# Kernel tuning notes

Measured on AMD Instinct MI355X. Metric: run time of the kernel, lower is better.

Reference implementation:

```python
import math
import jax, jax.numpy as jnp
import numpy as np

N_HEADS = 8

def setup_inputs() -> dict:
    key = jax.random.key(0)
    bs, n_heads, ch, l = 4, N_HEADS, 64, 1024
    width = 3 * n_heads * ch      # 1536 (packed q,k,v channels)
    T = 3 * l                     # 3072 (three spatial bands: ll, lh, hl)
    qkv = jax.random.normal(key, (bs, width, T), dtype=jnp.float32)
    return {"qkv": qkv, "l": l}

def reference(qkv, l):
    n_heads = N_HEADS
    bs, width, T = qkv.shape
    ch = width // (3 * n_heads)
    q, k, v = jnp.split(qkv, 3, axis=1)              # each (bs, n_heads*ch, T)
    scale = 1.0 / math.sqrt(math.sqrt(ch))
    qh = (q * scale).reshape(bs * n_heads, ch, T)
    kh = (k * scale).reshape(bs * n_heads, ch, T)
    vh = v.reshape(bs * n_heads, ch, T)
    # The original computes attention separately for q[:, :, :l], [l:2l], [2l:],
    # but k/v (and the softmax axis s) are identical, so computing attention
    # over the full query once and splitting the output is the same math.
    attn = jnp.einsum('bct,bcs->bts', qh, kh)        # (bs*H, T, T)
    w = jax.nn.softmax(attn.astype(jnp.float32), axis=-1).astype(attn.dtype)
    agg = jnp.einsum('bts,bcs->bct', w, vh).reshape(bs, n_heads * ch, T)
    return (agg[:, :, :l], agg[:, :, l:2 * l], agg[:, :, 2 * l:])
```

## Files before the change

### kernel.cpp

```cpp
#include <hip/hip_runtime.h>
#include <hip/hip_bf16.h>
#include <stdint.h>

#define T      3072
#define CH     64
#define HEADS  32
#define BM     128
#define BN     64
#define NIT    (T / BN)
#define PSTR   72

typedef unsigned short u16;
typedef short short8 __attribute__((ext_vector_type(8)));
typedef float floatx4 __attribute__((ext_vector_type(4)));

__device__ __forceinline__ unsigned pk2(float a, float b) {
  union { __hip_bfloat162 h; unsigned u; } cv;
  cv.h = __float22bfloat162_rn(float2{a, b});
  return cv.u;
}

__device__ __forceinline__ void gl_lds16(const void* g, void* l) {
  __builtin_amdgcn_global_load_lds(
      (const __attribute__((address_space(1))) uint32_t*)g,
      (__attribute__((address_space(3))) uint32_t*)l, 16, 0, 0);
}

__global__ __launch_bounds__(256) void qktrans(
    const float* __restrict__ qkv, u16* __restrict__ Qt, u16* __restrict__ Kt) {
  __shared__ __align__(16) u16 tl[64][PSTR];
  const int ttile = blockIdx.x, hh = blockIdx.y, role = blockIdx.z;
  const int b = hh >> 3, h = hh & 7;
  const int t0 = ttile * 64;
  const int tid = threadIdx.x;
  const float* src = qkv + (size_t)(b * 1536 + role * 512 + h * CH) * T;
  const float scale = (role == 0) ? 0.18033688011112042f : 1.0f;

#pragma unroll
  for (int p = 0; p < 2; ++p) {
    const int c0 = p * 32 + ((tid >> 4) << 1);
    const int ts = (tid & 15) * 4;
    float4 a = *(const float4*)(src + (size_t)c0 * T + t0 + ts);
    float4 c = *(const float4*)(src + (size_t)(c0 + 1) * T + t0 + ts);
    *(unsigned*)&tl[ts + 0][c0] = pk2(a.x * scale, c.x * scale);
    *(unsigned*)&tl[ts + 1][c0] = pk2(a.y * scale, c.y * scale);
    *(unsigned*)&tl[ts + 2][c0] = pk2(a.z * scale, c.z * scale);
    *(unsigned*)&tl[ts + 3][c0] = pk2(a.w * scale, c.w * scale);
  }
  __syncthreads();
  u16* dst = (role == 0 ? Qt : Kt) + (size_t)hh * T * CH;
#pragma unroll
  for (int q = 0; q < 2; ++q) {
    const int t = q * 32 + (tid >> 3);
    const int cc = (tid & 7) * 8;
    uint4 v = *(const uint4*)&tl[t][cc];
    *(uint4*)(dst + (size_t)(t0 + t) * CH + cc) = v;
  }
}

__global__ __launch_bounds__(256) void vcast(
    const float* __restrict__ qkv, u16* __restrict__ Vo) {
  const int b = blockIdx.y;
  const size_t i = ((size_t)blockIdx.x * 256 + threadIdx.x) * 8;
  const float4* s4 = (const float4*)(qkv + (size_t)b * 1536 * T + (size_t)1024 * T + i);
  float4 a = s4[0], c = s4[1];
  uint4 o;
  o.x = pk2(a.x, a.y); o.y = pk2(a.z, a.w);
  o.z = pk2(c.x, c.y); o.w = pk2(c.z, c.w);
  *(uint4*)(Vo + (size_t)b * 512 * T + i) = o;
}

__global__ __launch_bounds__(256, 3) void attn(
    const u16* __restrict__ Qt, const u16* __restrict__ Kt,
    const u16* __restrict__ Vg, float* __restrict__ out) {
  __shared__ __align__(16) u16 KB[2][BN * CH];
  __shared__ __align__(16) u16 VB[2][CH * BN];
  __shared__ __align__(16) u16 PL[4][32 * PSTR];

  const int qtile = blockIdx.x, hh = blockIdx.y;
  const int tid = threadIdx.x;
  const int wave = tid >> 6, lane = tid & 63;
  const int l15 = lane & 15, quad = lane >> 4;
  const int t0 = qtile * BM + wave * 32;

  const u16* Qh = Qt + (size_t)hh * T * CH;
  const u16* Kh = Kt + (size_t)hh * T * CH;
  const u16* Vh = Vg + (size_t)hh * CH * T;

  short8 qf[2][2];
#pragma unroll
  for (int tq = 0; tq < 2; ++tq)
#pragma unroll
    for (int kc = 0; kc < 2; ++kc)
      qf[tq][kc] = *(const short8*)(Qh + (size_t)(t0 + tq * 16 + l15) * CH + kc * 32 + quad * 8);

  floatx4 oacc[2][4] = {};
  float lsum[2][2] = {};

  int srow[2], scb[2];
#pragma unroll
  for (int j = 0; j < 2; ++j) {
    const int p = wave * 128 + j * 64 + lane;
    srow[j] = p >> 3;
    scb[j]  = (p & 7) ^ ((srow[j] + 2 * (srow[j] >> 3)) & 7);
  }
  const int swl = (l15 + 2 * (l15 >> 3)) & 7;
  u16* plw = PL[wave];

#define STAGE(buf, s0)                                                              \
  do {                                                                              \
    _Pragma("unroll")                                                               \
    for (int j = 0; j < 2; ++j)                                                     \
      gl_lds16(Kh + (size_t)((s0) + srow[j]) * CH + scb[j] * 8,                     \
               &KB[buf][(wave * 128 + j * 64) * 8]);                                \
    _Pragma("unroll")                                                               \
    for (int j = 0; j < 2; ++j)                                                     \
      gl_lds16(Vh + (size_t)srow[j] * T + (s0) + scb[j] * 8,                        \
               &VB[buf][(wave * 128 + j * 64) * 8]);                                \
  } while (0)

  STAGE(0, 0);

  for (int it = 0; it < NIT; ++it) {
    const int cur = it & 1;
    __syncthreads();
    if (it + 1 < NIT) STAGE(cur ^ 1, (it + 1) * BN);

    const u16* KL = KB[cur];
    const u16* VL = VB[cur];

    floatx4 sacc[2][4];
#pragma unroll
    for (int nt = 0; nt < 4; ++nt) {
      const int ph0 = quad ^ swl ^ ((nt & 1) * 4);
      const int base = (nt * 16 + l15) * CH;
      const short8 kf0 = *(const short8*)(KL + base + ph0 * 8);
      const short8 kf1 = *(const short8*)(KL + base + (ph0 ^ 4) * 8);
#pragma unroll
      for (int tq = 0; tq < 2; ++tq) {
        floatx4 z = {0.f, 0.f, 0.f, 0.f};
        z = __builtin_amdgcn_mfma_f32_16x16x32_bf16(kf0, qf[tq][0], z, 0, 0, 0);
        z = __builtin_amdgcn_mfma_f32_16x16x32_bf16(kf1, qf[tq][1], z, 0, 0, 0);
        sacc[tq][nt] = z;
      }
    }

#pragma unroll
    for (int tq = 0; tq < 2; ++tq)
#pragma unroll
      for (int nt = 0; nt < 4; ++nt) {
        floatx4 sv = sacc[tq][nt];
        float p0 = __builtin_amdgcn_exp2f(sv[0]);
        float p1 = __builtin_amdgcn_exp2f(sv[1]);
        float p2 = __builtin_amdgcn_exp2f(sv[2]);
        float p3 = __builtin_amdgcn_exp2f(sv[3]);
        lsum[tq][nt & 1] += (p0 + p1) + (p2 + p3);
        uint2 w; w.x = pk2(p0, p1); w.y = pk2(p2, p3);
        *(uint2*)(plw + (l15 + tq * 16) * PSTR + nt * 16 + quad * 4) = w;
      }

#pragma unroll
    for (int ks = 0; ks < 2; ++ks) {
      short8 pf0 = *(const short8*)(plw + l15 * PSTR + ks * 32 + quad * 8);
      short8 pf1 = *(const short8*)(plw + (l15 + 16) * PSTR + ks * 32 + quad * 8);
#pragma unroll
      for (int mt = 0; mt < 4; ++mt) {
        const int ph = quad ^ swl ^ ((mt & 1) * 4) ^ (ks * 4);
        const short8 vf = *(const short8*)(VL + (mt * 16 + l15) * BN + ph * 8);
        oacc[0][mt] = __builtin_amdgcn_mfma_f32_16x16x32_bf16(pf0, vf, oacc[0][mt], 0, 0, 0);
        oacc[1][mt] = __builtin_amdgcn_mfma_f32_16x16x32_bf16(pf1, vf, oacc[1][mt], 0, 0, 0);
      }
    }
  }

  float ls[2];
#pragma unroll
  for (int tq = 0; tq < 2; ++tq) {
    float s = lsum[tq][0] + lsum[tq][1];
    s += __shfl_xor(s, 16, 64);
    s += __shfl_xor(s, 32, 64);
    ls[tq] = s;
  }
  float linv[2][4];
#pragma unroll
  for (int tq = 0; tq < 2; ++tq)
#pragma unroll
    for (int r = 0; r < 4; ++r)
      linv[tq][r] = 1.0f / __shfl(ls[tq], quad * 4 + r, 64);

  const int b = hh >> 3, h = hh & 7;
#pragma unroll
  for (int tq = 0; tq < 2; ++tq) {
    const int tg = t0 + tq * 16 + quad * 4;
    const int band = tg >> 10, tt = tg & 1023;
    float* obase = out + (size_t)band * (4 * 512 * 1024)
                       + (size_t)b * (512 * 1024)
                       + (size_t)(h * CH) * 1024 + tt;
#pragma unroll
    for (int mt = 0; mt < 4; ++mt) {
      const int c = mt * 16 + l15;
      float4 v;
      v.x = oacc[tq][mt][0] * linv[tq][0];
      v.y = oacc[tq][mt][1] * linv[tq][1];
      v.z = oacc[tq][mt][2] * linv[tq][2];
      v.w = oacc[tq][mt][3] * linv[tq][3];
      *(float4*)(obase + (size_t)c * 1024) = v;
    }
  }
}

extern "C" void kernel_launch(void* const* d_in, const int* in_sizes, int n_in,
                              void* d_out, int out_size, void* d_ws, size_t ws_size,
                              hipStream_t stream) {
  (void)in_sizes; (void)n_in; (void)out_size; (void)ws_size;
  const float* qkv = (const float*)d_in[0];
  u16* Qt = (u16*)d_ws;
  u16* Kt = Qt + (size_t)HEADS * T * CH;
  u16* Vo = Kt + (size_t)HEADS * T * CH;
  float* out = (float*)d_out;

  qktrans<<<dim3(T / 64, HEADS, 2), 256, 0, stream>>>(qkv, Qt, Kt);
  vcast<<<dim3(768, 4), 256, 0, stream>>>(qkv, Vo);
  attn<<<dim3(T / BM, HEADS), 256, 0, stream>>>(Qt, Kt, Vo, out);
}
```

Baseline: 220.4 us.

## Keep softmax probabilities in registers via permlane swaps and fuse V cast

The exponentiated scores are packed to bf16 and rearranged across lanes with permlane32/permlane16 swaps to form the MFMA A-operand directly. This removes the per-iteration write and read of P through shared memory and drops the PL buffer. Separately, the V fp32-to-bf16 cast is folded into the Q/K transpose kernel as a third grid role, saving one launch. The register remap must match the MFMA operand layout exactly, and the swaps add cross-lane instructions.

```diff
diff --git a/kernel.cpp b/kernel.cpp
--- a/kernel.cpp
+++ b/kernel.cpp
@@ -8,7 +8,6 @@
 #define BM     128
 #define BN     64
 #define NIT    (T / BN)
-#define PSTR   72
 
 typedef unsigned short u16;
 typedef short short8 __attribute__((ext_vector_type(8)));
@@ -26,13 +25,49 @@
       (__attribute__((address_space(3))) uint32_t*)l, 16, 0, 0);
 }
 
+__device__ __forceinline__ void pl32swap(unsigned& x, unsigned& y) {
+#if __has_builtin(__builtin_amdgcn_permlane32_swap)
+  auto r = __builtin_amdgcn_permlane32_swap(x, y, false, false);
+  x = r[0]; y = r[1];
+#else
+  asm("v_permlane32_swap_b32 %0, %1" : "+v"(x), "+v"(y));
+#endif
+}
+__device__ __forceinline__ void pl16swap(unsigned& x, unsigned& y) {
+#if __has_builtin(__builtin_amdgcn_permlane16_swap)
+  auto r = __builtin_amdgcn_permlane16_swap(x, y, false, false);
+  x = r[0]; y = r[1];
+#else
+  asm("v_permlane16_swap_b32 %0, %1" : "+v"(x), "+v"(y));
+#endif
+}
+
 __global__ __launch_bounds__(256) void qktrans(
-    const float* __restrict__ qkv, u16* __restrict__ Qt, u16* __restrict__ Kt) {
-  __shared__ __align__(16) u16 tl[64][PSTR];
+    const float* __restrict__ qkv, u16* __restrict__ Qt, u16* __restrict__ Kt,
+    u16* __restrict__ Vo) {
+  __shared__ __align__(16) u16 tl[64][72];
   const int ttile = blockIdx.x, hh = blockIdx.y, role = blockIdx.z;
   const int b = hh >> 3, h = hh & 7;
   const int t0 = ttile * 64;
   const int tid = threadIdx.x;
+
+  if (role == 2) {
+    const float* vsrc = qkv + (size_t)(b * 1536 + 1024 + h * CH) * T;
+    u16* vdst = Vo + (size_t)(b * 512 + h * CH) * T;
+#pragma unroll
+    for (int p = 0; p < 2; ++p) {
+      const int r = p * 32 + (tid >> 3);
+      const int off = (tid & 7) * 8;
+      const float4* s4 = (const float4*)(vsrc + (size_t)r * T + t0 + off);
+      float4 a = s4[0], c = s4[1];
+      uint4 o;
+      o.x = pk2(a.x, a.y); o.y = pk2(a.z, a.w);
+      o.z = pk2(c.x, c.y); o.w = pk2(c.z, c.w);
+      *(uint4*)(vdst + (size_t)r * T + t0 + off) = o;
+    }
+    return;
+  }
+
   const float* src = qkv + (size_t)(b * 1536 + role * 512 + h * CH) * T;
   const float scale = (role == 0) ? 0.18033688011112042f : 1.0f;
 
@@ -58,24 +93,11 @@
   }
 }
 
-__global__ __launch_bounds__(256) void vcast(
-    const float* __restrict__ qkv, u16* __restrict__ Vo) {
-  const int b = blockIdx.y;
-  const size_t i = ((size_t)blockIdx.x * 256 + threadIdx.x) * 8;
-  const float4* s4 = (const float4*)(qkv + (size_t)b * 1536 * T + (size_t)1024 * T + i);
-  float4 a = s4[0], c = s4[1];
-  uint4 o;
-  o.x = pk2(a.x, a.y); o.y = pk2(a.z, a.w);
-  o.z = pk2(c.x, c.y); o.w = pk2(c.z, c.w);
-  *(uint4*)(Vo + (size_t)b * 512 * T + i) = o;
-}
-
 __global__ __launch_bounds__(256, 3) void attn(
     const u16* __restrict__ Qt, const u16* __restrict__ Kt,
     const u16* __restrict__ Vg, float* __restrict__ out) {
   __shared__ __align__(16) u16 KB[2][BN * CH];
   __shared__ __align__(16) u16 VB[2][CH * BN];
-  __shared__ __align__(16) u16 PL[4][32 * PSTR];
 
   const int qtile = blockIdx.x, hh = blockIdx.y;
   const int tid = threadIdx.x;
@@ -105,7 +127,6 @@
     scb[j]  = (p & 7) ^ ((srow[j] + 2 * (srow[j] >> 3)) & 7);
   }
   const int swl = (l15 + 2 * (l15 >> 3)) & 7;
-  u16* plw = PL[wave];
 
 #define STAGE(buf, s0)                                                              \
   do {                                                                              \
@@ -145,6 +166,7 @@
       }
     }
 
+    unsigned Apk[2][4], Bpk[2][4];
 #pragma unroll
     for (int tq = 0; tq < 2; ++tq)
 #pragma unroll
@@ -155,20 +177,29 @@
         float p2 = __builtin_amdgcn_exp2f(sv[2]);
         float p3 = __builtin_amdgcn_exp2f(sv[3]);
         lsum[tq][nt & 1] += (p0 + p1) + (p2 + p3);
-        uint2 w; w.x = pk2(p0, p1); w.y = pk2(p2, p3);
-        *(uint2*)(plw + (l15 + tq * 16) * PSTR + nt * 16 + quad * 4) = w;
+        Apk[tq][nt] = pk2(p0, p1);
+        Bpk[tq][nt] = pk2(p2, p3);
       }
 
 #pragma unroll
     for (int ks = 0; ks < 2; ++ks) {
-      short8 pf0 = *(const short8*)(plw + l15 * PSTR + ks * 32 + quad * 8);
-      short8 pf1 = *(const short8*)(plw + (l15 + 16) * PSTR + ks * 32 + quad * 8);
+      short8 pf[2];
+#pragma unroll
+      for (int tq = 0; tq < 2; ++tq) {
+        unsigned a0 = Apk[tq][2 * ks], a1 = Apk[tq][2 * ks + 1];
+        unsigned b0 = Bpk[tq][2 * ks], b1 = Bpk[tq][2 * ks + 1];
+        pl32swap(a0, a1); pl16swap(a0, a1);
+        pl32swap(b0, b1); pl16swap(b0, b1);
+        union { uint4 u; short8 s; } pw;
+        pw.u.x = a0; pw.u.y = b0; pw.u.z = a1; pw.u.w = b1;
+        pf[tq] = pw.s;
+      }
 #pragma unroll
       for (int mt = 0; mt < 4; ++mt) {
         const int ph = quad ^ swl ^ ((mt & 1) * 4) ^ (ks * 4);
         const short8 vf = *(const short8*)(VL + (mt * 16 + l15) * BN + ph * 8);
-        oacc[0][mt] = __builtin_amdgcn_mfma_f32_16x16x32_bf16(pf0, vf, oacc[0][mt], 0, 0, 0);
-        oacc[1][mt] = __builtin_amdgcn_mfma_f32_16x16x32_bf16(pf1, vf, oacc[1][mt], 0, 0, 0);
+        oacc[0][mt] = __builtin_amdgcn_mfma_f32_16x16x32_bf16(pf[0], vf, oacc[0][mt], 0, 0, 0);
+        oacc[1][mt] = __builtin_amdgcn_mfma_f32_16x16x32_bf16(pf[1], vf, oacc[1][mt], 0, 0, 0);
       }
     }
   }
@@ -219,7 +250,6 @@
   u16* Vo = Kt + (size_t)HEADS * T * CH;
   float* out = (float*)d_out;
 
-  qktrans<<<dim3(T / 64, HEADS, 2), 256, 0, stream>>>(qkv, Qt, Kt);
-  vcast<<<dim3(768, 4), 256, 0, stream>>>(qkv, Vo);
+  qktrans<<<dim3(T / 64, HEADS, 3), 256, 0, stream>>>(qkv, Qt, Kt, Vo);
   attn<<<dim3(T / BM, HEADS), 256, 0, stream>>>(Qt, Kt, Vo, out);
 }
```

Result: no change. 218.5 us (-0.9%).
